# Kernel tuning notes

Hardware: AMD Instinct MI355X
Metric: run time of the kernel (lower is better)

The kernel has to match this reference:

```python
import jax, jax.numpy as jnp
import numpy as np

B, S, D, H = 2, 2048, 1024, 16
DK = D // H

def setup_inputs() -> dict:
    key = jax.random.key(0)
    ks = jax.random.split(key, 12)
    def lin(k, shape, fan_in):
        bound = 1.0 / np.sqrt(fan_in)
        return jax.random.uniform(k, shape, jnp.float32, -bound, bound)
    inp = {
        'Q': jax.random.normal(ks[0], (B, S, D), jnp.float32),
        'K': jax.random.normal(ks[1], (B, S, D), jnp.float32),
        'V': jax.random.normal(ks[2], (B, S, D), jnp.float32),
        # padding mask: last 128 key positions of batch element 0 are padding
        'padding_mask': jnp.ones((B, 1, 1, S), jnp.int32).at[0, :, :, -128:].set(0),
        # causal look-ahead mask
        'look_ahead_mask': jnp.tril(jnp.ones((S, S), jnp.int32))[None, None],
        'Wq': lin(ks[3], (D, D), D), 'bq': lin(ks[4], (D,), D),
        'Wk': lin(ks[5], (D, D), D), 'bk': lin(ks[6], (D,), D),
        'Wv': lin(ks[7], (D, D), D), 'bv': lin(ks[8], (D,), D),
        'Wo': lin(ks[9], (D, D), D), 'bo': lin(ks[10], (D,), D),
    }
    return inp

def _split_heads(x):
    # [B,S,D] -> [B,H,S,DK]
    b, s, _ = x.shape
    return x.reshape(b, s, H, DK).transpose(0, 2, 1, 3)

def reference(Q, K, V, padding_mask, look_ahead_mask, Wq, bq, Wk, bk, Wv, bv, Wo, bo):
    q = _split_heads(Q @ Wq.T + bq)  # [B,H,S,DK]
    k = _split_heads(K @ Wk.T + bk)
    v = _split_heads(V @ Wv.T + bv)
    scores = jnp.einsum('bhqd,bhkd->bhqk', q, k) / np.sqrt(DK).astype(np.float32)
    neg_inf = jnp.float32(-jnp.inf)
    scores = jnp.where(padding_mask == 0, neg_inf, scores)
    scores = jnp.where(look_ahead_mask == 0, neg_inf, scores)
    weights = jax.nn.softmax(scores, axis=-1)  # dropout is identity in eval mode
    x = jnp.einsum('bhqk,bhkd->bhqd', weights, v)  # [B,H,S,DK]
    x = x.transpose(0, 2, 1, 3).reshape(Q.shape[0], Q.shape[1], D)
    return x @ Wo.T + bo
```

## Files before the change

kernel.cpp:

```cpp
#include <hip/hip_runtime.h>
#include <hip/hip_bf16.h>

#define B_   2
#define S_   2048
#define D_   1024
#define H_   16
#define DK_  64

typedef unsigned short u16;
typedef __attribute__((ext_vector_type(8))) short bf16x8;
typedef __attribute__((ext_vector_type(4))) float f32x4;

#define QSCALE   0.18033688011112042f
#define SMBIAS  -8.656170245333781f

static __device__ __forceinline__ u16 f2bf(float f) {
  union { float f; unsigned u; } v; v.f = f;
  unsigned r = v.u + 0x7FFF + ((v.u >> 16) & 1);
  return (u16)(r >> 16);
}

static __device__ __forceinline__ void gl_lds16(const void* g, void* l) {
  __builtin_amdgcn_global_load_lds(
      (const __attribute__((address_space(1))) void*)g,
      (__attribute__((address_space(3))) void*)l, 16, 0, 0);
}

__global__ void cvt_all(const float4* __restrict__ s0, const float4* __restrict__ s1,
                        const float4* __restrict__ s2, const float4* __restrict__ s3,
                        const float4* __restrict__ s4, const float4* __restrict__ s5,
                        const float4* __restrict__ s6,
                        ushort4* __restrict__ d0, ushort4* __restrict__ d1,
                        ushort4* __restrict__ d2, ushort4* __restrict__ d3,
                        ushort4* __restrict__ d4, ushort4* __restrict__ d5,
                        ushort4* __restrict__ d6, int nbig, int nsmall) {
  int y = blockIdx.y;
  const float4* in; ushort4* out; int n;
  switch (y) {
    case 0: in = s0; out = d0; n = nbig; break;
    case 1: in = s1; out = d1; n = nbig; break;
    case 2: in = s2; out = d2; n = nbig; break;
    case 3: in = s3; out = d3; n = nsmall; break;
    case 4: in = s4; out = d4; n = nsmall; break;
    case 5: in = s5; out = d5; n = nsmall; break;
    default: in = s6; out = d6; n = nsmall; break;
  }
  int i = blockIdx.x * blockDim.x + threadIdx.x;
  if (i < n) {
    float4 v = in[i];
    ushort4 r;
    r.x = f2bf(v.x); r.y = f2bf(v.y); r.z = f2bf(v.z); r.w = f2bf(v.w);
    out[i] = r;
  }
}

__launch_bounds__(256, 4)
__global__ void gemm_qkv(const u16* __restrict__ Xq, const u16* __restrict__ Xk, const u16* __restrict__ Xv,
                         const u16* __restrict__ Wq, const u16* __restrict__ Wk, const u16* __restrict__ Wv,
                         const float* __restrict__ bq, const float* __restrict__ bk, const float* __restrict__ bv,
                         u16* __restrict__ outq, u16* __restrict__ outk, u16* __restrict__ outv) {
  const int z = blockIdx.z;
  const int bid = blockIdx.x;
  const u16* Am; const u16* Bm; int m0, n0;
  if (z == 2)      { Am = Wv; Bm = Xv; m0 = (bid >> 6) * 128; n0 = (bid & 63) * 64; }
  else if (z == 1) { Am = Xk; Bm = Wk; m0 = (bid >> 4) * 128; n0 = (bid & 15) * 64; }
  else             { Am = Xq; Bm = Wq; m0 = (bid >> 4) * 128; n0 = (bid & 15) * 64; }
  const float* bias = (z == 0) ? bq : (z == 1) ? bk : bv;

  __shared__ __align__(16) u16 As[128 * 32];
  __shared__ __align__(16) u16 Bs[64 * 32];

  const int tid = threadIdx.x, lane = tid & 63, w = tid >> 6;
  const int q = lane >> 4, cl = lane & 15;

  f32x4 acc[2][4] = {};

  for (int k0 = 0; k0 < D_; k0 += 32) {
#pragma unroll
    for (int i = 0; i < 2; ++i) {
      int s = (i * 4 + w) * 64 + lane;
      int row = s >> 2, ko = (s & 3) << 3;
      gl_lds16(Am + (size_t)(m0 + row) * D_ + k0 + ko, As + (size_t)s * 8);
    }
    {
      int s = tid;
      int row = s >> 2, ko = (s & 3) << 3;
      gl_lds16(Bm + (size_t)(n0 + row) * D_ + k0 + ko, Bs + (size_t)s * 8);
    }
    __syncthreads();

    bf16x8 af[2], bfr[4];
#pragma unroll
    for (int r = 0; r < 2; ++r) af[r]  = *(const bf16x8*)(As + (w * 32 + r * 16 + cl) * 32 + q * 8);
#pragma unroll
    for (int c = 0; c < 4; ++c) bfr[c] = *(const bf16x8*)(Bs + (c * 16 + cl) * 32 + q * 8);
#pragma unroll
    for (int r = 0; r < 2; ++r)
#pragma unroll
      for (int c = 0; c < 4; ++c)
        acc[r][c] = __builtin_amdgcn_mfma_f32_16x16x32_bf16(af[r], bfr[c], acc[r][c], 0, 0, 0);
    __syncthreads();
  }

  if (z == 2) {
#pragma unroll
    for (int r = 0; r < 2; ++r) {
#pragma unroll
      for (int rr = 0; rr < 4; ++rr) {
        int j = m0 + w * 32 + r * 16 + q * 4 + rr;
        float bval = bias[j];
        int hh = j >> 6, dk = j & 63;
#pragma unroll
        for (int c = 0; c < 4; ++c) {
          int n = n0 + c * 16 + cl;
          int bb = n >> 11, s = n & (S_ - 1);
          outv[((size_t)(bb * H_ + hh) * DK_ + dk) * S_ + s] = f2bf(acc[r][c][rr] + bval);
        }
      }
    }
  } else {
    const float scale = (z == 0) ? QSCALE : 1.0f;
    u16* o = (z == 0) ? outq : outk;
#pragma unroll
    for (int c = 0; c < 4; ++c) {
      int j = n0 + c * 16 + cl;
      float bval = bias[j];
      int hh = j >> 6, dk = j & 63;
#pragma unroll
      for (int r = 0; r < 2; ++r) {
#pragma unroll
        for (int rr = 0; rr < 4; ++rr) {
          int n = m0 + w * 32 + r * 16 + q * 4 + rr;
          int bb = n >> 11, s = n & (S_ - 1);
          o[((size_t)(bb * H_ + hh) * S_ + s) * DK_ + dk] = f2bf((acc[r][c][rr] + bval) * scale);
        }
      }
    }
  }
}

__launch_bounds__(256, 2)
__global__ void attn(const u16* __restrict__ qh, const u16* __restrict__ kh,
                     const u16* __restrict__ vt, const int* __restrict__ pad,
                     u16* __restrict__ attn_out) {
  __shared__ __align__(16) u16 Ks[64 * 64];
  __shared__ __align__(16) u16 Vs[64 * 64];
  __shared__ __align__(16) u16 Ps[4][16 * 72];
  __shared__ float Kbias[64];

  const int tid = threadIdx.x, lane = tid & 63, w = tid >> 6;
  const int q = lane >> 4, cl = lane & 15;
  const int qt = (int)gridDim.x - 1 - (int)blockIdx.x;
  const int qb = qt * 64, h = blockIdx.y, b = blockIdx.z;

  const u16* Q = qh + (size_t)(b * H_ + h) * S_ * DK_;
  const u16* K = kh + (size_t)(b * H_ + h) * S_ * DK_;
  const u16* V = vt + (size_t)(b * H_ + h) * DK_ * S_;
  const int* pm = pad + b * S_;

  const int qr0 = qb + w * 16;
  bf16x8 qf0 = *(const bf16x8*)(Q + (qr0 + cl) * DK_ + q * 8);
  bf16x8 qf1 = *(const bf16x8*)(Q + (qr0 + cl) * DK_ + 32 + q * 8);

  f32x4 o[4] = {};
  float ls[4] = {0.f, 0.f, 0.f, 0.f};
  u16* Pw = Ps[w];

  const int nkv = qt + 1;
  for (int it = 0; it < nkv; ++it) {
    const int kb = it << 6;
#pragma unroll
    for (int i = 0; i < 2; ++i) {
      int s = (i * 4 + w) * 64 + lane;
      int row = s >> 3;
      int c = (s & 7) ^ (row & 7);
      gl_lds16(K + (size_t)(kb + row) * DK_ + (c << 3), Ks + (size_t)s * 8);
      gl_lds16(V + (size_t)row * S_ + kb + (c << 3), Vs + (size_t)s * 8);
    }
    if (tid < 64) {
      Kbias[tid] = (pm[kb + tid] != 0) ? SMBIAS : -3e38f;
    }
    __syncthreads();

    f32x4 sa[4];
#pragma unroll
    for (int ct = 0; ct < 4; ++ct) {
      int rk = ct * 16 + cl;
      int c0 = q ^ (rk & 7);
      bf16x8 kf0 = *(const bf16x8*)(Ks + rk * 64 + (c0 << 3));
      bf16x8 kf1 = *(const bf16x8*)(Ks + rk * 64 + ((c0 ^ 4) << 3));
      f32x4 zz = {};
      zz = __builtin_amdgcn_mfma_f32_16x16x32_bf16(qf0, kf0, zz, 0, 0, 0);
      zz = __builtin_amdgcn_mfma_f32_16x16x32_bf16(qf1, kf1, zz, 0, 0, 0);
      sa[ct] = zz;
    }

    if (it < qt) {
#pragma unroll
      for (int ct = 0; ct < 4; ++ct) {
        float kbv = Kbias[ct * 16 + cl];
#pragma unroll
        for (int rr = 0; rr < 4; ++rr) {
          float p = exp2f(sa[ct][rr] + kbv);
          ls[rr] += p;
          Pw[(q * 4 + rr) * 72 + ct * 16 + cl] = f2bf(p);
        }
      }
    } else {
#pragma unroll
      for (int ct = 0; ct < 4; ++ct) {
        int kg = kb + ct * 16 + cl;
        float kbv = Kbias[ct * 16 + cl];
#pragma unroll
        for (int rr = 0; rr < 4; ++rr) {
          int qg = qr0 + q * 4 + rr;
          float p = (kg <= qg) ? exp2f(sa[ct][rr] + kbv) : 0.f;
          ls[rr] += p;
          Pw[(q * 4 + rr) * 72 + ct * 16 + cl] = f2bf(p);
        }
      }
    }

    bf16x8 pf0 = *(const bf16x8*)(Pw + cl * 72 + q * 8);
    bf16x8 pf1 = *(const bf16x8*)(Pw + cl * 72 + 32 + q * 8);

#pragma unroll
    for (int ct = 0; ct < 4; ++ct) {
      int rv = ct * 16 + cl;
      int c0 = q ^ (rv & 7);
      bf16x8 vf0 = *(const bf16x8*)(Vs + rv * 64 + (c0 << 3));
      bf16x8 vf1 = *(const bf16x8*)(Vs + rv * 64 + ((c0 ^ 4) << 3));
      o[ct] = __builtin_amdgcn_mfma_f32_16x16x32_bf16(pf0, vf0, o[ct], 0, 0, 0);
      o[ct] = __builtin_amdgcn_mfma_f32_16x16x32_bf16(pf1, vf1, o[ct], 0, 0, 0);
    }
    __syncthreads();
  }

#pragma unroll
  for (int rr = 0; rr < 4; ++rr) {
    float l = ls[rr];
    l += __shfl_xor(l, 1, 64);
    l += __shfl_xor(l, 2, 64);
    l += __shfl_xor(l, 4, 64);
    l += __shfl_xor(l, 8, 64);
    float inv = 1.0f / l;
    int qg = qr0 + q * 4 + rr;
    size_t base = (size_t)(b * S_ + qg) * D_ + h * DK_;
#pragma unroll
    for (int ct = 0; ct < 4; ++ct)
      attn_out[base + ct * 16 + cl] = f2bf(o[ct][rr] * inv);
  }
}

__launch_bounds__(256, 4)
__global__ void gemm_out(const u16* __restrict__ A, const u16* __restrict__ W,
                         const float* __restrict__ bias, float* __restrict__ out) {
  __shared__ __align__(16) u16 As[128 * 32];
  __shared__ __align__(16) u16 Bs[64 * 32];

  const int tid = threadIdx.x, lane = tid & 63, w = tid >> 6;
  const int q = lane >> 4, cl = lane & 15;
  const int m0 = blockIdx.y * 128, n0 = blockIdx.x * 64;

  f32x4 acc[2][4] = {};

  for (int k0 = 0; k0 < D_; k0 += 32) {
#pragma unroll
    for (int i = 0; i < 2; ++i) {
      int s = (i * 4 + w) * 64 + lane;
      int row = s >> 2, ko = (s & 3) << 3;
      gl_lds16(A + (size_t)(m0 + row) * D_ + k0 + ko, As + (size_t)s * 8);
    }
    {
      int s = tid;
      int row = s >> 2, ko = (s & 3) << 3;
      gl_lds16(W + (size_t)(n0 + row) * D_ + k0 + ko, Bs + (size_t)s * 8);
    }
    __syncthreads();

    bf16x8 af[2], bfr[4];
#pragma unroll
    for (int r = 0; r < 2; ++r) af[r]  = *(const bf16x8*)(As + (w * 32 + r * 16 + cl) * 32 + q * 8);
#pragma unroll
    for (int c = 0; c < 4; ++c) bfr[c] = *(const bf16x8*)(Bs + (c * 16 + cl) * 32 + q * 8);
#pragma unroll
    for (int r = 0; r < 2; ++r)
#pragma unroll
      for (int c = 0; c < 4; ++c)
        acc[r][c] = __builtin_amdgcn_mfma_f32_16x16x32_bf16(af[r], bfr[c], acc[r][c], 0, 0, 0);
    __syncthreads();
  }

#pragma unroll
  for (int c = 0; c < 4; ++c) {
    int j = n0 + c * 16 + cl;
    float bval = bias[j];
#pragma unroll
    for (int r = 0; r < 2; ++r) {
#pragma unroll
      for (int rr = 0; rr < 4; ++rr) {
        int n = m0 + w * 32 + r * 16 + q * 4 + rr;
        out[(size_t)n * D_ + j] = acc[r][c][rr] + bval;
      }
    }
  }
}

extern "C" void kernel_launch(void* const* d_in, const int* in_sizes, int n_in,
                              void* d_out, int out_size, void* d_ws, size_t ws_size,
                              hipStream_t stream) {
  const float* Qf  = (const float*)d_in[0];
  const float* Kf  = (const float*)d_in[1];
  const float* Vf  = (const float*)d_in[2];
  const int*   pad = (const int*)d_in[3];
  const float* Wqf = (const float*)d_in[5];
  const float* bq  = (const float*)d_in[6];
  const float* Wkf = (const float*)d_in[7];
  const float* bk  = (const float*)d_in[8];
  const float* Wvf = (const float*)d_in[9];
  const float* bv  = (const float*)d_in[10];
  const float* Wof = (const float*)d_in[11];
  const float* bo  = (const float*)d_in[12];

  const size_t BSD = (size_t)B_ * S_ * D_;
  const size_t DD  = (size_t)D_ * D_;

  char* ws = (char*)d_ws;
  u16* Qb   = (u16*)ws; ws += BSD * 2;
  u16* Kb   = (u16*)ws; ws += BSD * 2;
  u16* Vb   = (u16*)ws; ws += BSD * 2;
  u16* Wqb  = (u16*)ws; ws += DD * 2;
  u16* Wkb  = (u16*)ws; ws += DD * 2;
  u16* Wvb  = (u16*)ws; ws += DD * 2;
  u16* Wob  = (u16*)ws; ws += DD * 2;
  u16* qhd  = (u16*)ws; ws += BSD * 2;
  u16* khd  = (u16*)ws; ws += BSD * 2;
  u16* vtd  = (u16*)ws; ws += BSD * 2;
  u16* attn_o = (u16*)ws; ws += BSD * 2;

  const int n4 = (int)(BSD / 4);
  const int w4 = (int)(DD / 4);
  dim3 gc(n4 / 256, 7);
  cvt_all<<<gc, 256, 0, stream>>>((const float4*)Qf, (const float4*)Kf, (const float4*)Vf,
                                  (const float4*)Wqf, (const float4*)Wkf, (const float4*)Wvf, (const float4*)Wof,
                                  (ushort4*)Qb, (ushort4*)Kb, (ushort4*)Vb,
                                  (ushort4*)Wqb, (ushort4*)Wkb, (ushort4*)Wvb, (ushort4*)Wob,
                                  n4, w4);

  dim3 g1(512, 1, 3);
  gemm_qkv<<<g1, 256, 0, stream>>>(Qb, Kb, Vb, Wqb, Wkb, Wvb, bq, bk, bv, qhd, khd, vtd);

  dim3 g2(S_ / 64, H_, B_);
  attn<<<g2, 256, 0, stream>>>(qhd, khd, vtd, pad, attn_o);

  dim3 g3(D_ / 64, (B_ * S_) / 128);
  gemm_out<<<g3, 256, 0, stream>>>(attn_o, Wob, bo, (float*)d_out);
}
```

Measured before the change: 273.8 us.

## Double-buffer LDS tiles in projection GEMMs and use grid-stride conversion kernel

Both projection GEMMs now use two LDS buffers: the next K-slice is fetched via global_load_lds into the other buffer while MFMAs run on the current one. This leaves one barrier per iteration instead of two and is meant to hide global-load latency. The conversion kernel becomes a grid-stride loop with a fixed 512x7 grid, so there are fewer blocks and many tiny weight-conversion blocks no longer exit early. Double buffering doubles LDS per block, which may limit occupancy. The code relies on the barrier ordering to ensure async LDS writes have completed before they are read.

```diff
diff --git a/kernel.cpp b/kernel.cpp
--- a/kernel.cpp
+++ b/kernel.cpp
@@ -45,8 +45,8 @@
     case 5: in = s5; out = d5; n = nsmall; break;
     default: in = s6; out = d6; n = nsmall; break;
   }
-  int i = blockIdx.x * blockDim.x + threadIdx.x;
-  if (i < n) {
+  const int stride = gridDim.x * blockDim.x;
+  for (int i = blockIdx.x * blockDim.x + threadIdx.x; i < n; i += stride) {
     float4 v = in[i];
     ushort4 r;
     r.x = f2bf(v.x); r.y = f2bf(v.y); r.z = f2bf(v.z); r.w = f2bf(v.w);
@@ -67,39 +67,57 @@
   else             { Am = Xq; Bm = Wq; m0 = (bid >> 4) * 128; n0 = (bid & 15) * 64; }
   const float* bias = (z == 0) ? bq : (z == 1) ? bk : bv;
 
-  __shared__ __align__(16) u16 As[128 * 32];
-  __shared__ __align__(16) u16 Bs[64 * 32];
+  __shared__ __align__(16) u16 As[2][128 * 32];
+  __shared__ __align__(16) u16 Bs[2][64 * 32];
 
   const int tid = threadIdx.x, lane = tid & 63, w = tid >> 6;
   const int q = lane >> 4, cl = lane & 15;
 
+#pragma unroll
+  for (int i = 0; i < 2; ++i) {
+    int s = (i * 4 + w) * 64 + lane;
+    int row = s >> 2, ko = (s & 3) << 3;
+    gl_lds16(Am + (size_t)(m0 + row) * D_ + ko, As[0] + (size_t)s * 8);
+  }
+  {
+    int s = tid;
+    int row = s >> 2, ko = (s & 3) << 3;
+    gl_lds16(Bm + (size_t)(n0 + row) * D_ + ko, Bs[0] + (size_t)s * 8);
+  }
+
   f32x4 acc[2][4] = {};
 
-  for (int k0 = 0; k0 < D_; k0 += 32) {
-#pragma unroll
-    for (int i = 0; i < 2; ++i) {
-      int s = (i * 4 + w) * 64 + lane;
-      int row = s >> 2, ko = (s & 3) << 3;
-      gl_lds16(Am + (size_t)(m0 + row) * D_ + k0 + ko, As + (size_t)s * 8);
-    }
-    {
-      int s = tid;
-      int row = s >> 2, ko = (s & 3) << 3;
-      gl_lds16(Bm + (size_t)(n0 + row) * D_ + k0 + ko, Bs + (size_t)s * 8);
-    }
+  for (int it = 0; it < 32; ++it) {
+    const int buf = it & 1;
     __syncthreads();
 
+    if (it < 31) {
+      const int k0 = (it + 1) * 32;
+#pragma unroll
+      for (int i = 0; i < 2; ++i) {
+        int s = (i * 4 + w) * 64 + lane;
+        int row = s >> 2, ko = (s & 3) << 3;
+        gl_lds16(Am + (size_t)(m0 + row) * D_ + k0 + ko, As[buf ^ 1] + (size_t)s * 8);
+      }
+      {
+        int s = tid;
+        int row = s >> 2, ko = (s & 3) << 3;
+        gl_lds16(Bm + (size_t)(n0 + row) * D_ + k0 + ko, Bs[buf ^ 1] + (size_t)s * 8);
+      }
+    }
+
+    const u16* At = As[buf];
+    const u16* Bt = Bs[buf];
     bf16x8 af[2], bfr[4];
 #pragma unroll
-    for (int r = 0; r < 2; ++r) af[r]  = *(const bf16x8*)(As + (w * 32 + r * 16 + cl) * 32 + q * 8);
-#pragma unroll
-    for (int c = 0; c < 4; ++c) bfr[c] = *(const bf16x8*)(Bs + (c * 16 + cl) * 32 + q * 8);
+    for (int r = 0; r < 2; ++r) af[r]  = *(const bf16x8*)(At + (w * 32 + r * 16 + cl) * 32 + q * 8);
+#pragma unroll
+    for (int c = 0; c < 4; ++c) bfr[c] = *(const bf16x8*)(Bt + (c * 16 + cl) * 32 + q * 8);
 #pragma unroll
     for (int r = 0; r < 2; ++r)
 #pragma unroll
       for (int c = 0; c < 4; ++c)
         acc[r][c] = __builtin_amdgcn_mfma_f32_16x16x32_bf16(af[r], bfr[c], acc[r][c], 0, 0, 0);
-    __syncthreads();
   }
 
   if (z == 2) {
@@ -255,40 +273,58 @@
 __launch_bounds__(256, 4)
 __global__ void gemm_out(const u16* __restrict__ A, const u16* __restrict__ W,
                          const float* __restrict__ bias, float* __restrict__ out) {
-  __shared__ __align__(16) u16 As[128 * 32];
-  __shared__ __align__(16) u16 Bs[64 * 32];
+  __shared__ __align__(16) u16 As[2][128 * 32];
+  __shared__ __align__(16) u16 Bs[2][64 * 32];
 
   const int tid = threadIdx.x, lane = tid & 63, w = tid >> 6;
   const int q = lane >> 4, cl = lane & 15;
   const int m0 = blockIdx.y * 128, n0 = blockIdx.x * 64;
 
+#pragma unroll
+  for (int i = 0; i < 2; ++i) {
+    int s = (i * 4 + w) * 64 + lane;
+    int row = s >> 2, ko = (s & 3) << 3;
+    gl_lds16(A + (size_t)(m0 + row) * D_ + ko, As[0] + (size_t)s * 8);
+  }
+  {
+    int s = tid;
+    int row = s >> 2, ko = (s & 3) << 3;
+    gl_lds16(W + (size_t)(n0 + row) * D_ + ko, Bs[0] + (size_t)s * 8);
+  }
+
   f32x4 acc[2][4] = {};
 
-  for (int k0 = 0; k0 < D_; k0 += 32) {
-#pragma unroll
-    for (int i = 0; i < 2; ++i) {
-      int s = (i * 4 + w) * 64 + lane;
-      int row = s >> 2, ko = (s & 3) << 3;
-      gl_lds16(A + (size_t)(m0 + row) * D_ + k0 + ko, As + (size_t)s * 8);
-    }
-    {
-      int s = tid;
-      int row = s >> 2, ko = (s & 3) << 3;
-      gl_lds16(W + (size_t)(n0 + row) * D_ + k0 + ko, Bs + (size_t)s * 8);
-    }
+  for (int it = 0; it < 32; ++it) {
+    const int buf = it & 1;
     __syncthreads();
 
+    if (it < 31) {
+      const int k0 = (it + 1) * 32;
+#pragma unroll
+      for (int i = 0; i < 2; ++i) {
+        int s = (i * 4 + w) * 64 + lane;
+        int row = s >> 2, ko = (s & 3) << 3;
+        gl_lds16(A + (size_t)(m0 + row) * D_ + k0 + ko, As[buf ^ 1] + (size_t)s * 8);
+      }
+      {
+        int s = tid;
+        int row = s >> 2, ko = (s & 3) << 3;
+        gl_lds16(W + (size_t)(n0 + row) * D_ + k0 + ko, Bs[buf ^ 1] + (size_t)s * 8);
+      }
+    }
+
+    const u16* At = As[buf];
+    const u16* Bt = Bs[buf];
     bf16x8 af[2], bfr[4];
 #pragma unroll
-    for (int r = 0; r < 2; ++r) af[r]  = *(const bf16x8*)(As + (w * 32 + r * 16 + cl) * 32 + q * 8);
-#pragma unroll
-    for (int c = 0; c < 4; ++c) bfr[c] = *(const bf16x8*)(Bs + (c * 16 + cl) * 32 + q * 8);
+    for (int r = 0; r < 2; ++r) af[r]  = *(const bf16x8*)(At + (w * 32 + r * 16 + cl) * 32 + q * 8);
+#pragma unroll
+    for (int c = 0; c < 4; ++c) bfr[c] = *(const bf16x8*)(Bt + (c * 16 + cl) * 32 + q * 8);
 #pragma unroll
     for (int r = 0; r < 2; ++r)
 #pragma unroll
       for (int c = 0; c < 4; ++c)
         acc[r][c] = __builtin_amdgcn_mfma_f32_16x16x32_bf16(af[r], bfr[c], acc[r][c], 0, 0, 0);
-    __syncthreads();
   }
 
 #pragma unroll
@@ -340,7 +376,7 @@
 
   const int n4 = (int)(BSD / 4);
   const int w4 = (int)(DD / 4);
-  dim3 gc(n4 / 256, 7);
+  dim3 gc(512, 7);
   cvt_all<<<gc, 256, 0, stream>>>((const float4*)Qf, (const float4*)Kf, (const float4*)Vf,
                                   (const float4*)Wqf, (const float4*)Wkf, (const float4*)Wvf, (const float4*)Wof,
                                   (ushort4*)Qb, (ushort4*)Kb, (ushort4*)Vb,
```

Result: no change. 268.5 us (-1.9%).
